# Optimization experiments

Hardware: AMD Instinct MI355X
Metric: run time of the kernel (lower is better)

The kernel has to match this reference:

```python
import jax, jax.numpy as jnp
import numpy as np
import math

H, DK, G_DIM, S_DIM, HID = 8, 64, 512, 3072, 512
B = 16384
EPS = 1e-5

def _layernorm(x, g, b):
    mu = jnp.mean(x, axis=-1, keepdims=True)
    var = jnp.mean((x - mu) ** 2, axis=-1, keepdims=True)
    return (x - mu) * jax.lax.rsqrt(var + EPS) * g + b

def setup_inputs() -> dict:
    key = jax.random.key(0)
    ks = jax.random.split(key, 12)
    s = 0.02
    return {
        "h_g": jax.random.normal(ks[0], (B, G_DIM), jnp.float32),
        "h_s": jax.random.normal(ks[1], (B, S_DIM), jnp.float32),
        # stacked per-head projections: [H, in_dim, d_k]
        "Wq": jax.random.normal(ks[2], (H, G_DIM, DK), jnp.float32) * s,
        "bq": jnp.zeros((H, DK), jnp.float32),
        "Wk": jax.random.normal(ks[3], (H, S_DIM, DK), jnp.float32) * s,
        "bk": jnp.zeros((H, DK), jnp.float32),
        "Wv": jax.random.normal(ks[4], (H, S_DIM, DK), jnp.float32) * s,
        "bv": jnp.zeros((H, DK), jnp.float32),
        "Wo": jax.random.normal(ks[5], (HID, HID), jnp.float32) * s,
        "bo": jnp.zeros((HID,), jnp.float32),
        "ln1_g": jnp.ones((HID,), jnp.float32),
        "ln1_b": jnp.zeros((HID,), jnp.float32),
        "W1": jax.random.normal(ks[6], (HID, 2 * HID), jnp.float32) * s,
        "b1": jnp.zeros((2 * HID,), jnp.float32),
        "W2": jax.random.normal(ks[7], (2 * HID, HID), jnp.float32) * s,
        "b2": jnp.zeros((HID,), jnp.float32),
        "ln2_g": jnp.ones((HID,), jnp.float32),
        "ln2_b": jnp.zeros((HID,), jnp.float32),
    }

def reference(h_g, h_s, Wq, bq, Wk, bk, Wv, bv, Wo, bo, ln1_g, ln1_b, W1, b1, W2, b2, ln2_g, ln2_b):
    b = h_g.shape[0]
    # batched per-head projections (fuses the per-head Linear loop)
    Q = jnp.einsum('bg,hgd->bhd', h_g, Wq) + bq          # [B,H,DK]
    K = jnp.einsum('bs,hsd->bhd', h_s, Wk) + bk          # [B,H,DK]
    V = jnp.einsum('bs,hsd->bhd', h_s, Wv) + bv          # [B,H,DK]
    # seq_len == 1: scores is [B,H,1]; softmax over a single key == 1
    scores = jnp.sum(Q * K, axis=-1, keepdims=True) / math.sqrt(DK)
    attn_w = jax.nn.softmax(scores, axis=-1)             # identically ones
    attn = attn_w * V                                    # == V
    h_concat = attn.reshape(b, H * DK)                   # [B,HID]
    h_attn = h_concat @ Wo + bo
    h_attn = _layernorm(h_attn + h_g, ln1_g, ln1_b)
    # MLP (dropout is identity in eval mode); torch GELU default = exact erf
    h = jax.nn.gelu(h_attn @ W1 + b1, approximate=False) @ W2 + b2
    return _layernorm(h + h_attn, ln2_g, ln2_b)
```

## Files before the change

kernel.cpp:

```cpp
#include <hip/hip_runtime.h>
#include <hip/hip_bf16.h>
#include <math.h>

#define HH    8
#define DKK   64
#define GD    512
#define SD    3072
#define HID_  512
#define BB    16384

typedef unsigned short ushort_t;
typedef __attribute__((ext_vector_type(8))) short bf16x8;
typedef __attribute__((ext_vector_type(4))) float f32x4;

__device__ __forceinline__ float bf2f(ushort_t u) {
  union { unsigned int i; float f; } c; c.i = ((unsigned int)u) << 16; return c.f;
}
__device__ __forceinline__ ushort_t f2bf(float f) {
  union { float f; unsigned int i; } c; c.f = f;
  unsigned int x = c.i;
  return (ushort_t)((x + 0x7FFFu + ((x >> 16) & 1u)) >> 16);
}
__device__ __forceinline__ unsigned int pk_bf16(float a, float b) {
  __hip_bfloat162 h = __float22bfloat162_rn(make_float2(a, b));
  union { __hip_bfloat162 h; unsigned int u; } c; c.h = h; return c.u;
}

__device__ __forceinline__ void async_cp16(const ushort_t* gsrc, ushort_t* ldst) {
  __builtin_amdgcn_global_load_lds(
      (const __attribute__((address_space(1))) unsigned int*)gsrc,
      (__attribute__((address_space(3))) unsigned int*)ldst, 16, 0, 0);
}
__device__ __forceinline__ void async_cp16f(const float* gsrc, float* ldst) {
  __builtin_amdgcn_global_load_lds(
      (const __attribute__((address_space(1))) unsigned int*)gsrc,
      (__attribute__((address_space(3))) unsigned int*)ldst, 16, 0, 0);
}

__device__ __forceinline__ float gelu_tanh(float x) {
  float y = 0.79788456080286535588f * (x + 0.044715f * x * x * x);
  float e = __expf(2.0f * y);
  float th = 1.0f - 2.0f / (e + 1.0f);
  return 0.5f * x * (1.0f + th);
}

__device__ __forceinline__ void swz_coords(int& nb, int& mb, int& kz) {
  int NB = gridDim.x, MB = gridDim.y;
  int bid = blockIdx.x + NB * (blockIdx.y + MB * blockIdx.z);
  int xcd = bid & 7;
  int j = bid >> 3;
  nb = j & (NB - 1);
  int rest = j / NB;
  int mk = (rest << 3) | xcd;
  mb = mk & (MB - 1);
  kz = mk / MB;
}

template <int EPI, int SWZ>
__global__ __launch_bounds__(256) void gemm_bt(
    const ushort_t* __restrict__ A, const ushort_t* __restrict__ Bt,
    void* __restrict__ Cv, const float* __restrict__ bias,
    int M, int N, int Kfull, int Klen) {
  __shared__ __align__(16) ushort_t As[2][128 * 32];
  __shared__ __align__(16) ushort_t Bs[2][128 * 32];
  const int tid = threadIdx.x;
  const int wv = tid >> 6;
  const int lane = tid & 63;
  int nb, mb, kz;
  if (SWZ) swz_coords(nb, mb, kz);
  else { nb = blockIdx.x; mb = blockIdx.y; kz = blockIdx.z; }
  const int m0 = mb * 128, n0 = nb * 128, kbeg = kz * Klen;
  const int srow = lane >> 2;
  const int scol = (lane & 3) * 8;
  const int wm = wv & 1, wn = wv >> 1;
  const int lr = lane & 15, quad = lane >> 4;

  f32x4 acc[4][4];
#pragma unroll
  for (int i = 0; i < 4; ++i)
#pragma unroll
    for (int j = 0; j < 4; ++j) acc[i][j] = (f32x4){0.f, 0.f, 0.f, 0.f};

  const ushort_t* Ab = A + (size_t)m0 * Kfull + kbeg;
  const ushort_t* Bb = Bt + (size_t)n0 * Kfull + kbeg;

  auto stage = [&](int k0, int b) {
#pragma unroll
    for (int i = 0; i < 2; ++i) {
      const int chunk = i * 4 + wv;
      const int row = chunk * 16 + srow;
      async_cp16(Ab + (size_t)row * Kfull + (k0 + scol), &As[b][chunk * 512]);
      async_cp16(Bb + (size_t)row * Kfull + (k0 + scol), &Bs[b][chunk * 512]);
    }
  };

  const int nt = Klen >> 5;
  stage(0, 0);
  int buf = 0;
  for (int t = 0; t < nt; ++t, buf ^= 1) {
    if (t + 1 < nt) {
      stage((t + 1) << 5, buf ^ 1);
      asm volatile("s_waitcnt vmcnt(4)" ::: "memory");
    } else {
      asm volatile("s_waitcnt vmcnt(0)" ::: "memory");
    }
    __builtin_amdgcn_s_barrier();
    __builtin_amdgcn_sched_barrier(0);
    bf16x8 af[4], bfr[4];
#pragma unroll
    for (int i = 0; i < 4; ++i)
      af[i] = *(const bf16x8*)&As[buf][(wm * 64 + i * 16 + lr) * 32 + quad * 8];
#pragma unroll
    for (int j = 0; j < 4; ++j)
      bfr[j] = *(const bf16x8*)&Bs[buf][(wn * 64 + j * 16 + lr) * 32 + quad * 8];
#pragma unroll
    for (int i = 0; i < 4; ++i)
#pragma unroll
      for (int j = 0; j < 4; ++j)
        acc[i][j] = __builtin_amdgcn_mfma_f32_16x16x32_bf16(af[i], bfr[j], acc[i][j], 0, 0, 0);
    __builtin_amdgcn_sched_barrier(0);
    __builtin_amdgcn_s_barrier();
  }

#pragma unroll
  for (int i = 0; i < 4; ++i) {
    const int mg = m0 + wm * 64 + i * 16 + quad * 4;
#pragma unroll
    for (int j = 0; j < 4; ++j) {
      const int ng = n0 + wn * 64 + j * 16 + lr;
      if (EPI == 2) {
        float* C = (float*)Cv + (size_t)kz * M * N;
#pragma unroll
        for (int r = 0; r < 4; ++r)
          C[(size_t)(mg + r) * N + ng] = acc[i][j][r];
      } else {
        ushort_t* C = (ushort_t*)Cv;
        const float bvv = bias ? bias[ng] : 0.0f;
#pragma unroll
        for (int r = 0; r < 4; ++r) {
          float v = acc[i][j][r] + bvv;
          if (EPI == 1) v = gelu_tanh(v);
          C[(size_t)(mg + r) * N + ng] = f2bf(v);
        }
      }
    }
  }
}

__global__ __launch_bounds__(256, 4) void gemm_a32(
    const float* __restrict__ A, const ushort_t* __restrict__ Bt,
    float* __restrict__ C, int M, int N, int Kfull, int Klen) {
  __shared__ __align__(16) float As4[2][128 * 32];
  __shared__ __align__(16) ushort_t Bs[2][128 * 32];
  const int tid = threadIdx.x;
  const int wv = tid >> 6;
  const int lane = tid & 63;
  int nb, mb, kz;
  swz_coords(nb, mb, kz);
  const int m0 = mb * 128, n0 = nb * 128, kbeg = kz * Klen;
  const int srow = lane >> 2;
  const int scol = (lane & 3) * 8;
  const int wm = wv & 1, wn = wv >> 1;
  const int lr = lane & 15, quad = lane >> 4;
  const int a_rc = lane >> 3;
  const int a_g = (lane & 7) ^ a_rc;

  f32x4 acc[4][4];
#pragma unroll
  for (int i = 0; i < 4; ++i)
#pragma unroll
    for (int j = 0; j < 4; ++j) acc[i][j] = (f32x4){0.f, 0.f, 0.f, 0.f};

  const float* Ab = A + (size_t)m0 * Kfull + kbeg;
  const ushort_t* Bb = Bt + (size_t)n0 * Kfull + kbeg;

  auto stage = [&](int k0, int b) {
#pragma unroll
    for (int i = 0; i < 2; ++i) {
      const int chunk = i * 4 + wv;
      const int row = chunk * 16 + srow;
      async_cp16(Bb + (size_t)row * Kfull + (k0 + scol), &Bs[b][chunk * 512]);
    }
#pragma unroll
    for (int t4 = 0; t4 < 4; ++t4) {
      const int chunkA = t4 * 4 + wv;
      const int r = chunkA * 8 + a_rc;
      async_cp16f(Ab + (size_t)r * Kfull + (k0 + 4 * a_g), &As4[b][chunkA * 256]);
    }
  };

  const int nt = Klen >> 5;
  stage(0, 0);
  int buf = 0;
  for (int t = 0; t < nt; ++t, buf ^= 1) {
    if (t + 1 < nt) {
      stage((t + 1) << 5, buf ^ 1);
      asm volatile("s_waitcnt vmcnt(6)" ::: "memory");
    } else {
      asm volatile("s_waitcnt vmcnt(0)" ::: "memory");
    }
    __builtin_amdgcn_s_barrier();
    __builtin_amdgcn_sched_barrier(0);
    bf16x8 af[4], bfr[4];
#pragma unroll
    for (int i = 0; i < 4; ++i) {
      const int r = wm * 64 + i * 16 + lr;
      const int x0 = (2 * quad) ^ (lr & 7);
      const int x1 = (2 * quad + 1) ^ (lr & 7);
      float4 fa = *(const float4*)&As4[buf][r * 32 + x0 * 4];
      float4 fb = *(const float4*)&As4[buf][r * 32 + x1 * 4];
      union { unsigned int u[4]; bf16x8 v; } c;
      c.u[0] = pk_bf16(fa.x, fa.y); c.u[1] = pk_bf16(fa.z, fa.w);
      c.u[2] = pk_bf16(fb.x, fb.y); c.u[3] = pk_bf16(fb.z, fb.w);
      af[i] = c.v;
    }
#pragma unroll
    for (int j = 0; j < 4; ++j)
      bfr[j] = *(const bf16x8*)&Bs[buf][(wn * 64 + j * 16 + lr) * 32 + quad * 8];
#pragma unroll
    for (int i = 0; i < 4; ++i)
#pragma unroll
      for (int j = 0; j < 4; ++j)
        acc[i][j] = __builtin_amdgcn_mfma_f32_16x16x32_bf16(af[i], bfr[j], acc[i][j], 0, 0, 0);
    __builtin_amdgcn_sched_barrier(0);
    __builtin_amdgcn_s_barrier();
  }

  float* Cp = C + (size_t)kz * M * N;
#pragma unroll
  for (int i = 0; i < 4; ++i) {
    const int mg = m0 + wm * 64 + i * 16 + quad * 4;
#pragma unroll
    for (int j = 0; j < 4; ++j) {
      const int ng = n0 + wn * 64 + j * 16 + lr;
#pragma unroll
      for (int r = 0; r < 4; ++r)
        Cp[(size_t)(mg + r) * N + ng] = acc[i][j][r];
    }
  }
}

__global__ __launch_bounds__(256) void permute_wv(const float* __restrict__ Wv,
                                                  ushort_t* __restrict__ Wvp) {
  const int idx = (blockIdx.x * 256 + threadIdx.x) * 8;
  const int s = idx >> 9;
  const int c = idx & 511;
  const float* src = Wv + (size_t)(c >> 6) * (SD * DKK) + (size_t)s * DKK + (c & 63);
  float4 a = *(const float4*)src;
  float4 b = *(const float4*)(src + 4);
  unsigned int p[4];
  p[0] = pk_bf16(a.x, a.y); p[1] = pk_bf16(a.z, a.w);
  p[2] = pk_bf16(b.x, b.y); p[3] = pk_bf16(b.z, b.w);
  *(uint4*)(Wvp + idx) = *(const uint4*)p;
}

__global__ __launch_bounds__(256) void transpose3(
    const float* __restrict__ s0, ushort_t* __restrict__ d0,
    const float* __restrict__ s1, ushort_t* __restrict__ d1,
    const float* __restrict__ s2, ushort_t* __restrict__ d2) {
  __shared__ ushort_t tile[32][33];
  const int z = blockIdx.z;
  const float* src = (z == 0) ? s0 : (z == 1) ? s1 : s2;
  ushort_t* dst = (z == 0) ? d0 : (z == 1) ? d1 : d2;
  const int R = (z == 2) ? 1024 : 512;
  const int C = (z == 1) ? 1024 : 512;
  const int bx = blockIdx.x * 32;
  const int by = blockIdx.y * 32;
  if (bx >= C || by >= R) return;
  const int tx = threadIdx.x, ty = threadIdx.y;
#pragma unroll
  for (int i = 0; i < 32; i += 8)
    tile[ty + i][tx] = f2bf(src[(size_t)(by + ty + i) * C + (bx + tx)]);
  __syncthreads();
#pragma unroll
  for (int i = 0; i < 32; i += 8)
    dst[(size_t)(bx + ty + i) * R + (by + tx)] = tile[tx][ty + i];
}

__global__ __launch_bounds__(256) void c0_kernel(const float* __restrict__ bv,
                                                 const float* __restrict__ Wo,
                                                 const float* __restrict__ bo,
                                                 float* __restrict__ c0) {
  __shared__ float red[8][32];
  const int jl = threadIdx.x & 31;
  const int chunk = threadIdx.x >> 5;
  const int j = blockIdx.x * 32 + jl;
  const int cbase = chunk * 64;
  float s = 0.f;
#pragma unroll 8
  for (int c = 0; c < 64; ++c) s += bv[cbase + c] * Wo[(size_t)(cbase + c) * 512 + j];
  red[chunk][jl] = s;
  __syncthreads();
  if (chunk == 0) {
    float t = bo[j];
#pragma unroll
    for (int q = 0; q < 8; ++q) t += red[q][jl];
    c0[j] = t;
  }
}

template <int RES_F32, int OUT_F32>
__global__ __launch_bounds__(256) void ln_fused(const float* __restrict__ p0,
                                                const float* __restrict__ p1,
                                                const float* __restrict__ cb,
                                                const void* __restrict__ res_,
                                                const float* __restrict__ g,
                                                const float* __restrict__ b,
                                                void* __restrict__ out_) {
  const int row = blockIdx.x * 4 + (threadIdx.x >> 6);
  const int lane = threadIdx.x & 63;
  const size_t base = (size_t)row * 512 + lane * 8;
  const int col = lane * 8;
  float4 a0 = *(const float4*)(p0 + base);
  float4 a1 = *(const float4*)(p0 + base + 4);
  float4 c0v = *(const float4*)(p1 + base);
  float4 c1v = *(const float4*)(p1 + base + 4);
  float4 d0 = *(const float4*)(cb + col);
  float4 d1 = *(const float4*)(cb + col + 4);
  float t[8];
  t[0] = a0.x + c0v.x + d0.x; t[1] = a0.y + c0v.y + d0.y;
  t[2] = a0.z + c0v.z + d0.z; t[3] = a0.w + c0v.w + d0.w;
  t[4] = a1.x + c1v.x + d1.x; t[5] = a1.y + c1v.y + d1.y;
  t[6] = a1.z + c1v.z + d1.z; t[7] = a1.w + c1v.w + d1.w;
  float r[8];
  if (RES_F32) {
    const float* res = (const float*)res_;
    float4 e0 = *(const float4*)(res + base);
    float4 e1 = *(const float4*)(res + base + 4);
    r[0] = e0.x; r[1] = e0.y; r[2] = e0.z; r[3] = e0.w;
    r[4] = e1.x; r[5] = e1.y; r[6] = e1.z; r[7] = e1.w;
  } else {
    const ushort_t* res = (const ushort_t*)res_;
    uint4 rv = *(const uint4*)(res + base);
    const ushort_t* rp = (const ushort_t*)&rv;
#pragma unroll
    for (int k = 0; k < 8; ++k) r[k] = bf2f(rp[k]);
  }
  float x[8];
  float s = 0.f, sq = 0.f;
#pragma unroll
  for (int k = 0; k < 8; ++k) {
    float v = t[k] + r[k];
    x[k] = v; s += v; sq += v * v;
  }
#pragma unroll
  for (int off = 32; off > 0; off >>= 1) {
    s += __shfl_xor(s, off);
    sq += __shfl_xor(sq, off);
  }
  const float mean = s * (1.0f / 512.0f);
  const float var = sq * (1.0f / 512.0f) - mean * mean;
  const float rstd = rsqrtf(var + 1e-5f);
  float4 gv0 = *(const float4*)(g + col);
  float4 gv1 = *(const float4*)(g + col + 4);
  float4 bv0 = *(const float4*)(b + col);
  float4 bv1 = *(const float4*)(b + col + 4);
  const float gg[8] = {gv0.x, gv0.y, gv0.z, gv0.w, gv1.x, gv1.y, gv1.z, gv1.w};
  const float bb[8] = {bv0.x, bv0.y, bv0.z, bv0.w, bv1.x, bv1.y, bv1.z, bv1.w};
  float y[8];
#pragma unroll
  for (int k = 0; k < 8; ++k) y[k] = (x[k] - mean) * rstd * gg[k] + bb[k];
  if (OUT_F32) {
    float* out = (float*)out_;
    *(float4*)(out + base) = make_float4(y[0], y[1], y[2], y[3]);
    *(float4*)(out + base + 4) = make_float4(y[4], y[5], y[6], y[7]);
  } else {
    ushort_t* out = (ushort_t*)out_;
    uint4 ov; ushort_t* op = (ushort_t*)&ov;
#pragma unroll
    for (int k = 0; k < 8; ++k) op[k] = f2bf(y[k]);
    *(uint4*)(out + base) = ov;
  }
}

extern "C" void kernel_launch(void* const* d_in, const int* in_sizes, int n_in,
                              void* d_out, int out_size, void* d_ws, size_t ws_size,
                              hipStream_t stream) {
  const float* h_g  = (const float*)d_in[0];
  const float* h_s  = (const float*)d_in[1];
  const float* Wv   = (const float*)d_in[6];
  const float* bv   = (const float*)d_in[7];
  const float* Wo   = (const float*)d_in[8];
  const float* bo   = (const float*)d_in[9];
  const float* ln1g = (const float*)d_in[10];
  const float* ln1b = (const float*)d_in[11];
  const float* W1   = (const float*)d_in[12];
  const float* b1   = (const float*)d_in[13];
  const float* W2   = (const float*)d_in[14];
  const float* b2   = (const float*)d_in[15];
  const float* ln2g = (const float*)d_in[16];
  const float* ln2b = (const float*)d_in[17];

  char* ws = (char*)d_ws;
  ushort_t* WoT = (ushort_t*)(ws + 0);
  ushort_t* W1T = (ushort_t*)(ws + 524288);
  ushort_t* W2T = (ushort_t*)(ws + 1572864);
  ushort_t* Wvp = (ushort_t*)(ws + 2621440);
  ushort_t* WcT = (ushort_t*)(ws + 5767168);
  float*    c0f = (float*)(ws + 8912896);
  float*    p0  = (float*)(ws + 16777216);
  float*    p1  = (float*)(ws + 50331648);
  ushort_t* x   = (ushort_t*)(ws + 83886080);
  ushort_t* u   = (ushort_t*)(ws + 100663296);
  float*    q0  = p0;
  float*    q1  = p1;
  (void)in_sizes; (void)n_in; (void)out_size; (void)ws_size;

  hipLaunchKernelGGL(permute_wv, dim3(768), dim3(256), 0, stream, Wv, Wvp);
  hipLaunchKernelGGL(transpose3, dim3(32, 32, 3), dim3(32, 8), 0, stream,
                     Wo, WoT, W1, W1T, W2, W2T);
  hipLaunchKernelGGL(c0_kernel, dim3(16), dim3(256), 0, stream, bv, Wo, bo, c0f);

  hipLaunchKernelGGL((gemm_bt<0, 0>), dim3(24, 4, 1), dim3(256), 0, stream,
                     WoT, Wvp, (void*)WcT, (const float*)nullptr, 512, 3072, 512, 512);
  hipLaunchKernelGGL(gemm_a32, dim3(4, 128, 2), dim3(256), 0, stream,
                     h_s, WcT, p0, BB, 512, 3072, 1536);
  hipLaunchKernelGGL((ln_fused<1, 0>), dim3(4096), dim3(256), 0, stream,
                     p0, p1, c0f, (const void*)h_g, ln1g, ln1b, (void*)x);
  hipLaunchKernelGGL((gemm_bt<1, 1>), dim3(8, 128, 1), dim3(256), 0, stream,
                     x, W1T, (void*)u, b1, BB, 1024, 512, 512);
  hipLaunchKernelGGL((gemm_bt<2, 1>), dim3(4, 128, 2), dim3(256), 0, stream,
                     u, W2T, (void*)q0, (const float*)nullptr, BB, 512, 1024, 512);
  hipLaunchKernelGGL((ln_fused<0, 1>), dim3(4096), dim3(256), 0, stream,
                     q0, q1, b2, (const void*)x, ln2g, ln2b, d_out);
}
```

Measured before the change: 557.9 us.

## Replace LDS-staged GEMMs with direct global-to-register MFMA GEMM

Adds a gemm_rd kernel in which each wave loads its A and B MFMA fragments straight from global memory into registers, with no LDS staging, double buffering or barriers. It replaces the fp32-A projection GEMM and both MLP GEMMs. The aim is to remove the LDS round-trip and barrier synchronisation. In exchange, data shared between waves is no longer reused through LDS, so each A/B row is fetched by two waves via cache. Loads are also no longer prefetched ahead of the MFMAs, which risks exposed memory latency.

```diff
diff --git a/kernel.cpp b/kernel.cpp
--- a/kernel.cpp
+++ b/kernel.cpp
@@ -27,11 +27,6 @@
 }
 
 __device__ __forceinline__ void async_cp16(const ushort_t* gsrc, ushort_t* ldst) {
-  __builtin_amdgcn_global_load_lds(
-      (const __attribute__((address_space(1))) unsigned int*)gsrc,
-      (__attribute__((address_space(3))) unsigned int*)ldst, 16, 0, 0);
-}
-__device__ __forceinline__ void async_cp16f(const float* gsrc, float* ldst) {
   __builtin_amdgcn_global_load_lds(
       (const __attribute__((address_space(1))) unsigned int*)gsrc,
       (__attribute__((address_space(3))) unsigned int*)ldst, 16, 0, 0);
@@ -54,6 +49,84 @@
   int mk = (rest << 3) | xcd;
   mb = mk & (MB - 1);
   kz = mk / MB;
+}
+
+template <int EPI, int AF32>
+__global__ __launch_bounds__(256, 4) void gemm_rd(
+    const void* __restrict__ Av, const ushort_t* __restrict__ Bt,
+    void* __restrict__ Cv, const float* __restrict__ bias,
+    int M, int N, int Kfull, int Klen) {
+  const int tid = threadIdx.x;
+  const int wv = tid >> 6;
+  const int lane = tid & 63;
+  int nb, mb, kz;
+  swz_coords(nb, mb, kz);
+  const int m0 = mb * 128, n0 = nb * 128, kbeg = kz * Klen;
+  const int wm = wv & 1, wn = wv >> 1;
+  const int lr = lane & 15, quad = lane >> 4;
+
+  f32x4 acc[4][4];
+#pragma unroll
+  for (int i = 0; i < 4; ++i)
+#pragma unroll
+    for (int j = 0; j < 4; ++j) acc[i][j] = (f32x4){0.f, 0.f, 0.f, 0.f};
+
+  const size_t rstep = (size_t)16 * Kfull;
+  const ushort_t* Bb = Bt + (size_t)(n0 + wn * 64 + lr) * Kfull + (kbeg + quad * 8);
+  const float* Abf = (const float*)Av + (size_t)(m0 + wm * 64 + lr) * Kfull + (kbeg + quad * 8);
+  const ushort_t* Abh = (const ushort_t*)Av + (size_t)(m0 + wm * 64 + lr) * Kfull + (kbeg + quad * 8);
+
+  for (int k0 = 0; k0 < Klen; k0 += 32) {
+    bf16x8 af[4], bfr[4];
+#pragma unroll
+    for (int j = 0; j < 4; ++j)
+      bfr[j] = *(const bf16x8*)(Bb + (size_t)j * rstep + k0);
+    if (AF32) {
+#pragma unroll
+      for (int i = 0; i < 4; ++i) {
+        const float* pa = Abf + (size_t)i * rstep + k0;
+        float4 fa = *(const float4*)pa;
+        float4 fb = *(const float4*)(pa + 4);
+        union { unsigned int u[4]; bf16x8 v; } c;
+        c.u[0] = pk_bf16(fa.x, fa.y); c.u[1] = pk_bf16(fa.z, fa.w);
+        c.u[2] = pk_bf16(fb.x, fb.y); c.u[3] = pk_bf16(fb.z, fb.w);
+        af[i] = c.v;
+      }
+    } else {
+#pragma unroll
+      for (int i = 0; i < 4; ++i)
+        af[i] = *(const bf16x8*)(Abh + (size_t)i * rstep + k0);
+    }
+#pragma unroll
+    for (int i = 0; i < 4; ++i)
+#pragma unroll
+      for (int j = 0; j < 4; ++j)
+        acc[i][j] = __builtin_amdgcn_mfma_f32_16x16x32_bf16(af[i], bfr[j], acc[i][j], 0, 0, 0);
+  }
+
+#pragma unroll
+  for (int i = 0; i < 4; ++i) {
+    const int mg = m0 + wm * 64 + i * 16 + quad * 4;
+#pragma unroll
+    for (int j = 0; j < 4; ++j) {
+      const int ng = n0 + wn * 64 + j * 16 + lr;
+      if (EPI == 2) {
+        float* C = (float*)Cv + (size_t)kz * M * N;
+#pragma unroll
+        for (int r = 0; r < 4; ++r)
+          C[(size_t)(mg + r) * N + ng] = acc[i][j][r];
+      } else {
+        ushort_t* C = (ushort_t*)Cv;
+        const float bvv = bias ? bias[ng] : 0.0f;
+#pragma unroll
+        for (int r = 0; r < 4; ++r) {
+          float v = acc[i][j][r] + bvv;
+          if (EPI == 1) v = gelu_tanh(v);
+          C[(size_t)(mg + r) * N + ng] = f2bf(v);
+        }
+      }
+    }
+  }
 }
 
 template <int EPI, int SWZ>
@@ -143,99 +216,6 @@
           C[(size_t)(mg + r) * N + ng] = f2bf(v);
         }
       }
-    }
-  }
-}
-
-__global__ __launch_bounds__(256, 4) void gemm_a32(
-    const float* __restrict__ A, const ushort_t* __restrict__ Bt,
-    float* __restrict__ C, int M, int N, int Kfull, int Klen) {
-  __shared__ __align__(16) float As4[2][128 * 32];
-  __shared__ __align__(16) ushort_t Bs[2][128 * 32];
-  const int tid = threadIdx.x;
-  const int wv = tid >> 6;
-  const int lane = tid & 63;
-  int nb, mb, kz;
-  swz_coords(nb, mb, kz);
-  const int m0 = mb * 128, n0 = nb * 128, kbeg = kz * Klen;
-  const int srow = lane >> 2;
-  const int scol = (lane & 3) * 8;
-  const int wm = wv & 1, wn = wv >> 1;
-  const int lr = lane & 15, quad = lane >> 4;
-  const int a_rc = lane >> 3;
-  const int a_g = (lane & 7) ^ a_rc;
-
-  f32x4 acc[4][4];
-#pragma unroll
-  for (int i = 0; i < 4; ++i)
-#pragma unroll
-    for (int j = 0; j < 4; ++j) acc[i][j] = (f32x4){0.f, 0.f, 0.f, 0.f};
-
-  const float* Ab = A + (size_t)m0 * Kfull + kbeg;
-  const ushort_t* Bb = Bt + (size_t)n0 * Kfull + kbeg;
-
-  auto stage = [&](int k0, int b) {
-#pragma unroll
-    for (int i = 0; i < 2; ++i) {
-      const int chunk = i * 4 + wv;
-      const int row = chunk * 16 + srow;
-      async_cp16(Bb + (size_t)row * Kfull + (k0 + scol), &Bs[b][chunk * 512]);
-    }
-#pragma unroll
-    for (int t4 = 0; t4 < 4; ++t4) {
-      const int chunkA = t4 * 4 + wv;
-      const int r = chunkA * 8 + a_rc;
-      async_cp16f(Ab + (size_t)r * Kfull + (k0 + 4 * a_g), &As4[b][chunkA * 256]);
-    }
-  };
-
-  const int nt = Klen >> 5;
-  stage(0, 0);
-  int buf = 0;
-  for (int t = 0; t < nt; ++t, buf ^= 1) {
-    if (t + 1 < nt) {
-      stage((t + 1) << 5, buf ^ 1);
-      asm volatile("s_waitcnt vmcnt(6)" ::: "memory");
-    } else {
-      asm volatile("s_waitcnt vmcnt(0)" ::: "memory");
-    }
-    __builtin_amdgcn_s_barrier();
-    __builtin_amdgcn_sched_barrier(0);
-    bf16x8 af[4], bfr[4];
-#pragma unroll
-    for (int i = 0; i < 4; ++i) {
-      const int r = wm * 64 + i * 16 + lr;
-      const int x0 = (2 * quad) ^ (lr & 7);
-      const int x1 = (2 * quad + 1) ^ (lr & 7);
-      float4 fa = *(const float4*)&As4[buf][r * 32 + x0 * 4];
-      float4 fb = *(const float4*)&As4[buf][r * 32 + x1 * 4];
-      union { unsigned int u[4]; bf16x8 v; } c;
-      c.u[0] = pk_bf16(fa.x, fa.y); c.u[1] = pk_bf16(fa.z, fa.w);
-      c.u[2] = pk_bf16(fb.x, fb.y); c.u[3] = pk_bf16(fb.z, fb.w);
-      af[i] = c.v;
-    }
-#pragma unroll
-    for (int j = 0; j < 4; ++j)
-      bfr[j] = *(const bf16x8*)&Bs[buf][(wn * 64 + j * 16 + lr) * 32 + quad * 8];
-#pragma unroll
-    for (int i = 0; i < 4; ++i)
-#pragma unroll
-      for (int j = 0; j < 4; ++j)
-        acc[i][j] = __builtin_amdgcn_mfma_f32_16x16x32_bf16(af[i], bfr[j], acc[i][j], 0, 0, 0);
-    __builtin_amdgcn_sched_barrier(0);
-    __builtin_amdgcn_s_barrier();
-  }
-
-  float* Cp = C + (size_t)kz * M * N;
-#pragma unroll
-  for (int i = 0; i < 4; ++i) {
-    const int mg = m0 + wm * 64 + i * 16 + quad * 4;
-#pragma unroll
-    for (int j = 0; j < 4; ++j) {
-      const int ng = n0 + wn * 64 + j * 16 + lr;
-#pragma unroll
-      for (int r = 0; r < 4; ++r)
-        Cp[(size_t)(mg + r) * N + ng] = acc[i][j][r];
     }
   }
 }
@@ -413,14 +393,16 @@
 
   hipLaunchKernelGGL((gemm_bt<0, 0>), dim3(24, 4, 1), dim3(256), 0, stream,
                      WoT, Wvp, (void*)WcT, (const float*)nullptr, 512, 3072, 512, 512);
-  hipLaunchKernelGGL(gemm_a32, dim3(4, 128, 2), dim3(256), 0, stream,
-                     h_s, WcT, p0, BB, 512, 3072, 1536);
+  hipLaunchKernelGGL((gemm_rd<2, 1>), dim3(4, 128, 2), dim3(256), 0, stream,
+                     (const void*)h_s, WcT, (void*)p0, (const float*)nullptr,
+                     BB, 512, 3072, 1536);
   hipLaunchKernelGGL((ln_fused<1, 0>), dim3(4096), dim3(256), 0, stream,
                      p0, p1, c0f, (const void*)h_g, ln1g, ln1b, (void*)x);
-  hipLaunchKernelGGL((gemm_bt<1, 1>), dim3(8, 128, 1), dim3(256), 0, stream,
-                     x, W1T, (void*)u, b1, BB, 1024, 512, 512);
-  hipLaunchKernelGGL((gemm_bt<2, 1>), dim3(4, 128, 2), dim3(256), 0, stream,
-                     u, W2T, (void*)q0, (const float*)nullptr, BB, 512, 1024, 512);
+  hipLaunchKernelGGL((gemm_rd<1, 0>), dim3(8, 128, 1), dim3(256), 0, stream,
+                     (const void*)x, W1T, (void*)u, b1, BB, 1024, 512, 512);
+  hipLaunchKernelGGL((gemm_rd<2, 0>), dim3(4, 128, 2), dim3(256), 0, stream,
+                     (const void*)u, W2T, (void*)q0, (const float*)nullptr,
+                     BB, 512, 1024, 512);
   hipLaunchKernelGGL((ln_fused<0, 1>), dim3(4096), dim3(256), 0, stream,
                      q0, q1, b2, (const void*)x, ln2g, ln2b, d_out);
 }
```

New measurement: 735.9 us. +31.9%, slower.
